# Kernel optimization log

Hardware: AMD Instinct MI355X
Metric: run time of the kernel (lower is better)

Reference implementation:

```python
import jax, jax.numpy as jnp
import numpy as np
from jax import lax

B, T, I, H, O, L = 32, 1024, 128, 512, 128, 2


def _lstm_layer(x, Wih, Whh, bih, bhh):
    # x: [B, T, in]; Wih: [4H, in]; Whh: [4H, H]; PyTorch gate order i,f,g,o
    Hs = Whh.shape[1]
    # Precompute input contribution for all timesteps (one big GEMM)
    xg = jnp.einsum('bti,gi->btg', x, Wih) + bih + bhh  # [B, T, 4H]
    xg_t = jnp.swapaxes(xg, 0, 1)  # [T, B, 4H] for scan

    def step(carry, g_in):
        h, c = carry
        g = g_in + h @ Whh.T  # [B, 4H]
        i, f, gg, o = jnp.split(g, 4, axis=-1)
        i = jax.nn.sigmoid(i)
        f = jax.nn.sigmoid(f)
        gg = jnp.tanh(gg)
        o = jax.nn.sigmoid(o)
        c = f * c + i * gg
        h = o * jnp.tanh(c)
        return (h, c), h

    h0 = jnp.zeros((x.shape[0], Hs), dtype=x.dtype)
    c0 = jnp.zeros((x.shape[0], Hs), dtype=x.dtype)
    (_, _), hs = lax.scan(step, (h0, c0), xg_t)
    return jnp.swapaxes(hs, 0, 1)  # [B, T, H]


def setup_inputs() -> dict:
    key = jax.random.key(0)
    ks = jax.random.split(key, 16)
    s = 1.0 / np.sqrt(H)  # torch LSTM/Linear init scale
    u = lambda k, shape: jax.random.uniform(k, shape, jnp.float32, -s, s)
    return {
        'x': jax.random.normal(ks[0], (B, T, I), jnp.float32),
        'W_ih0': u(ks[1], (4 * H, I)), 'W_hh0': u(ks[2], (4 * H, H)),
        'b_ih0': u(ks[3], (4 * H,)), 'b_hh0': u(ks[4], (4 * H,)),
        'W_ih1': u(ks[5], (4 * H, H)), 'W_hh1': u(ks[6], (4 * H, H)),
        'b_ih1': u(ks[7], (4 * H,)), 'b_hh1': u(ks[8], (4 * H,)),
        'fcW': u(ks[9], (O, H)), 'fcb': u(ks[10], (O,)),
        'fc2W': jax.random.uniform(ks[11], (O, O), jnp.float32, -1.0 / np.sqrt(O), 1.0 / np.sqrt(O)),
        'fc2b': jax.random.uniform(ks[12], (O,), jnp.float32, -1.0 / np.sqrt(O), 1.0 / np.sqrt(O)),
    }


def reference(x, W_ih0, W_hh0, b_ih0, b_hh0, W_ih1, W_hh1, b_ih1, b_hh1, fcW, fcb, fc2W, fc2b):
    h1 = _lstm_layer(x, W_ih0, W_hh0, b_ih0, b_hh0)   # [B, T, H]
    h2 = _lstm_layer(h1, W_ih1, W_hh1, b_ih1, b_hh1)  # [B, T, H]
    out = h2 @ fcW.T + fcb    # [B, T, O]
    out2 = out @ fc2W.T + fc2b  # [B, T, O]
    return out2
```

## Files before the change

### kernel.cpp

```cpp
#include <hip/hip_runtime.h>
#include <math.h>

typedef _Float16 f16;
typedef _Float16 f16x8 __attribute__((ext_vector_type(8)));
typedef _Float16 f16x4 __attribute__((ext_vector_type(4)));
typedef _Float16 f16x2 __attribute__((ext_vector_type(2)));
typedef float f32x16 __attribute__((ext_vector_type(16)));
typedef int i32x4 __attribute__((ext_vector_type(4)));

#define B_ 32
#define T_ 1024
#define I_ 128
#define H_ 512

#define NWG 64
#define THR 512

#define OFF_FLAGS 0UL
#define OFF_H1S   4096UL
#define OFF_H2S   33591296UL
#define OFF_XT    67178496UL

__device__ inline f32x16 mfma32(f16x8 a, f16x8 b, f32x16 c) {
  return __builtin_amdgcn_mfma_f32_32x32x16_f16(a, b, c, 0, 0, 0);
}
__device__ inline float fast_sig(float x) { return 1.f / (1.f + __expf(-x)); }
__device__ inline float fast_tanh(float x) {
  float e = __expf(-2.f * fabsf(x));
  float t = (1.f - e) / (1.f + e);
  return x < 0.f ? -t : t;
}

__device__ inline unsigned ld_sc1_u32(const unsigned* p) {
  unsigned r;
  asm volatile("global_load_dword %0, %1, off sc1\n\ts_waitcnt vmcnt(0)"
               : "=v"(r) : "v"(p) : "memory");
  return r;
}
__device__ inline void st_sc1_u32(unsigned* p, unsigned v) {
  asm volatile("global_store_dword %0, %1, off sc1" :: "v"(p), "v"(v) : "memory");
}

__device__ inline int swz_h(int b, int kbyte) { return b * 1024 + (kbyte ^ ((b & 7) << 4)); }
__device__ inline int swz_x(int b, int kbyte) { return b * 256  + (kbyte ^ ((b & 7) << 4)); }

__global__ __launch_bounds__(256) void prep_xT(const float* __restrict__ x, f16* __restrict__ xT) {
  const int idx = blockIdx.x * 256 + threadIdx.x;
  const int n4 = B_ * T_ * I_ / 4;
  if (idx < n4) {
    const int i4 = idx * 4;
    const int i  = i4 & (I_ - 1);
    const int tt = (i4 >> 7) & (T_ - 1);
    const int b  = i4 >> 17;
    float4 v = *(const float4*)(x + i4);
    f16x4 o;
    o[0] = (f16)v.x; o[1] = (f16)v.y; o[2] = (f16)v.z; o[3] = (f16)v.w;
    *(f16x4*)(xT + ((size_t)tt * B_ + b) * I_ + i) = o;
  }
}

__global__ __launch_bounds__(THR, 1) void lstm_persist(
    const float* __restrict__ Wih0, const float* __restrict__ Whh0,
    const float* __restrict__ bih0, const float* __restrict__ bhh0,
    const float* __restrict__ Wih1, const float* __restrict__ Whh1,
    const float* __restrict__ bih1, const float* __restrict__ bhh1,
    char* ws) {
  __shared__ i32x4 h1l4[2048];
  __shared__ i32x4 h2l4[2048];
  __shared__ i32x4 xl4[512];
  __shared__ float gbuf[2 * 32 * 68];
  __shared__ float biasl[64];

  const int tid  = threadIdx.x;
  const int wgid = blockIdx.x;
  const int role = wgid >> 5;
  const int gid  = wgid & 31;
  const int lane = tid & 63;
  const int wv   = tid >> 6;
  const int nt   = wv & 1;
  const int kq   = (wv >> 1) & 1;
  const int bl   = lane & 31;
  const int kg   = lane >> 5;

  unsigned* flags0 = (unsigned*)(ws + OFF_FLAGS);
  unsigned* flags1 = (unsigned*)(ws + OFF_FLAGS + 2048);
  const char* h1base = ws + OFF_H1S;
  const char* h2base = ws + OFF_H2S;

  if (tid < 64) {
    const int g = tid >> 4, hc = tid & 15;
    const int row = g * 512 + gid * 16 + hc;
    biasl[tid] = role ? (bih1[row] + bhh1[row]) : (bih0[row] + bhh0[row]);
  }

  const int n    = nt * 32 + bl;
  const int wrow = (n >> 4) * 512 + gid * 16 + (n & 15);
  f16x8 wreg[32];
  if (role == 0) {
    if (wv < 4) {
#pragma unroll
      for (int ks = 0; ks < 20; ++ks) {
        const int k = kq * 320 + ks * 16 + kg * 8;
        const float* src = (k < I_) ? (Wih0 + (size_t)wrow * I_ + k)
                                    : (Whh0 + (size_t)wrow * H_ + (k - I_));
        float4 v0 = *(const float4*)(src);
        float4 v1 = *(const float4*)(src + 4);
        f16x8 h;
        h[0] = (f16)v0.x; h[1] = (f16)v0.y; h[2] = (f16)v0.z; h[3] = (f16)v0.w;
        h[4] = (f16)v1.x; h[5] = (f16)v1.y; h[6] = (f16)v1.z; h[7] = (f16)v1.w;
        wreg[ks] = h;
      }
    }
  } else {
    if (wv < 4) {
#pragma unroll
      for (int ks = 0; ks < 32; ++ks) {
        const int k = kq * 512 + ks * 16 + kg * 8;
        const float* src = (k < H_) ? (Wih1 + (size_t)wrow * H_ + k)
                                    : (Whh1 + (size_t)wrow * H_ + (k - H_));
        float4 v0 = *(const float4*)(src);
        float4 v1 = *(const float4*)(src + 4);
        f16x8 h;
        h[0] = (f16)v0.x; h[1] = (f16)v0.y; h[2] = (f16)v0.z; h[3] = (f16)v0.w;
        h[4] = (f16)v1.x; h[5] = (f16)v1.y; h[6] = (f16)v1.z; h[7] = (f16)v1.w;
        wreg[ks] = h;
      }
    }
  }

  float cst0 = 0.f, cst1 = 0.f;
  const char* h1c = (const char*)h1l4;
  const char* h2c = (const char*)h2l4;
  const char* xc  = (const char*)xl4;

  __syncthreads();

  if (role == 0) {
    for (int s = 0; s < T_; ++s) {
      i32x4 xv = ((const i32x4*)(ws + OFF_XT))[(size_t)s * 512 + tid];

      if (s >= 1) {
        if (tid < 64) {
          const unsigned tgt = (unsigned)s;
          const unsigned* fp = flags0 + (tid < 32 ? tid : 0) * 16;
          const bool active = tid < 32;
          for (;;) {
            unsigned v = ld_sc1_u32(fp);
            if (!active) v = tgt;
            if (__all((int)(v >= tgt))) break;
            __builtin_amdgcn_s_sleep(1);
          }
        }
        __syncthreads();
      }

      {
        const i32x4* src = (const i32x4*)(h1base + (size_t)s * 32768);
#pragma unroll
        for (int r = 0; r < 4; ++r) {
          const int u = r * 512 + tid;
          i32x4 v = src[u];
          const int wgs = u >> 6, b = (u >> 1) & 31, half = u & 1;
          *(i32x4*)((char*)h1l4 + swz_h(b, wgs * 32 + half * 16)) = v;
        }
      }
      *(i32x4*)((char*)xl4 + swz_x(tid >> 4, (tid & 15) * 16)) = xv;
      __syncthreads();

      if (wv < 4) {
        f32x16 acc = {};
        if (kq == 0) {
#pragma unroll
          for (int ks = 0; ks < 8; ++ks) {
            f16x8 a = *(const f16x8*)(xc + swz_x(bl, (ks * 16 + kg * 8) * 2));
            acc = mfma32(a, wreg[ks], acc);
          }
#pragma unroll
          for (int ks = 8; ks < 20; ++ks) {
            f16x8 a = *(const f16x8*)(h1c + swz_h(bl, (ks * 16 + kg * 8 - I_) * 2));
            acc = mfma32(a, wreg[ks], acc);
          }
        } else {
#pragma unroll
          for (int ks = 0; ks < 20; ++ks) {
            f16x8 a = *(const f16x8*)(h1c + swz_h(bl, (192 + ks * 16 + kg * 8) * 2));
            acc = mfma32(a, wreg[ks], acc);
          }
        }
        const int cb = nt * 32 + bl;
#pragma unroll
        for (int r = 0; r < 16; ++r) {
          const int row = (r & 3) + 8 * (r >> 2) + 4 * kg;
          gbuf[kq * 2176 + row * 68 + cb] = acc[r];
        }
      }
      __syncthreads();

      if (tid < 256) {
        const int rb = tid >> 3, hp = tid & 7;
        const float* gr = gbuf + rb * 68;
        float hv[2];
#pragma unroll
        for (int cc = 0; cc < 2; ++cc) {
          const int c = 2 * hp + cc;
          const float pi = gr[c]      + gr[2176 + c]      + biasl[c];
          const float pf = gr[16 + c] + gr[2176 + 16 + c] + biasl[16 + c];
          const float pg = gr[32 + c] + gr[2176 + 32 + c] + biasl[32 + c];
          const float po = gr[48 + c] + gr[2176 + 48 + c] + biasl[48 + c];
          const float ig = fast_sig(pi), fg = fast_sig(pf);
          const float gg = fast_tanh(pg), og = fast_sig(po);
          const float cprev = cc ? cst1 : cst0;
          const float cnew = fg * cprev + ig * gg;
          if (cc) cst1 = cnew; else cst0 = cnew;
          hv[cc] = og * fast_tanh(cnew);
        }
        f16x2 pk; pk[0] = (f16)hv[0]; pk[1] = (f16)hv[1];
        unsigned* dst = (unsigned*)(h1base + (size_t)(s + 1) * 32768 +
                                    (size_t)gid * 1024 + rb * 32 + hp * 4);
        st_sc1_u32(dst, __builtin_bit_cast(unsigned, pk));
      }

      asm volatile("s_waitcnt vmcnt(0)" ::: "memory");
      __syncthreads();
      if (tid == 0) st_sc1_u32(flags0 + gid * 16, (unsigned)(s + 1));
      __builtin_amdgcn_sched_barrier(0);
    }
  } else {
    for (int t = 0; t < T_; ++t) {
      if (tid < 64) {
        const unsigned tgt = (unsigned)(t + 1);
        const unsigned* fp = flags0 + (tid < 32 ? tid : 0) * 16;
        const bool active = tid < 32;
        for (;;) {
          unsigned v = ld_sc1_u32(fp);
          if (!active) v = tgt;
          if (__all((int)(v >= tgt))) break;
          __builtin_amdgcn_s_sleep(1);
        }
      }
      __syncthreads();

      {
        const i32x4* src = (const i32x4*)(h1base + (size_t)(t + 1) * 32768);
#pragma unroll
        for (int r = 0; r < 4; ++r) {
          const int u = r * 512 + tid;
          i32x4 v = src[u];
          const int wgs = u >> 6, b = (u >> 1) & 31, half = u & 1;
          *(i32x4*)((char*)h1l4 + swz_h(b, wgs * 32 + half * 16)) = v;
        }
      }

      if (t >= 1) {
        if (tid < 64) {
          const unsigned tgt = (unsigned)t;
          const unsigned* fp = flags1 + (tid < 32 ? tid : 0) * 16;
          const bool active = tid < 32;
          for (;;) {
            unsigned v = ld_sc1_u32(fp);
            if (!active) v = tgt;
            if (__all((int)(v >= tgt))) break;
            __builtin_amdgcn_s_sleep(1);
          }
        }
      }
      __syncthreads();

      {
        const i32x4* src = (const i32x4*)(h2base + (size_t)t * 32768);
#pragma unroll
        for (int r = 0; r < 4; ++r) {
          const int u = r * 512 + tid;
          i32x4 v = src[u];
          const int wgs = u >> 6, b = (u >> 1) & 31, half = u & 1;
          *(i32x4*)((char*)h2l4 + swz_h(b, wgs * 32 + half * 16)) = v;
        }
      }
      __syncthreads();

      if (wv < 4) {
        f32x16 acc = {};
        if (kq == 0) {
#pragma unroll
          for (int ks = 0; ks < 32; ++ks) {
            f16x8 a = *(const f16x8*)(h1c + swz_h(bl, (ks * 16 + kg * 8) * 2));
            acc = mfma32(a, wreg[ks], acc);
          }
        } else {
#pragma unroll
          for (int ks = 0; ks < 32; ++ks) {
            f16x8 a = *(const f16x8*)(h2c + swz_h(bl, (ks * 16 + kg * 8) * 2));
            acc = mfma32(a, wreg[ks], acc);
          }
        }
        const int cb = nt * 32 + bl;
#pragma unroll
        for (int r = 0; r < 16; ++r) {
          const int row = (r & 3) + 8 * (r >> 2) + 4 * kg;
          gbuf[kq * 2176 + row * 68 + cb] = acc[r];
        }
      }
      __syncthreads();

      if (tid < 256) {
        const int rb = tid >> 3, hp = tid & 7;
        const float* gr = gbuf + rb * 68;
        float hv[2];
#pragma unroll
        for (int cc = 0; cc < 2; ++cc) {
          const int c = 2 * hp + cc;
          const float pi = gr[c]      + gr[2176 + c]      + biasl[c];
          const float pf = gr[16 + c] + gr[2176 + 16 + c] + biasl[16 + c];
          const float pg = gr[32 + c] + gr[2176 + 32 + c] + biasl[32 + c];
          const float po = gr[48 + c] + gr[2176 + 48 + c] + biasl[48 + c];
          const float ig = fast_sig(pi), fg = fast_sig(pf);
          const float gg = fast_tanh(pg), og = fast_sig(po);
          const float cprev = cc ? cst1 : cst0;
          const float cnew = fg * cprev + ig * gg;
          if (cc) cst1 = cnew; else cst0 = cnew;
          hv[cc] = og * fast_tanh(cnew);
        }
        f16x2 pk; pk[0] = (f16)hv[0]; pk[1] = (f16)hv[1];
        unsigned* dst = (unsigned*)(h2base + (size_t)(t + 1) * 32768 +
                                    (size_t)gid * 1024 + rb * 32 + hp * 4);
        st_sc1_u32(dst, __builtin_bit_cast(unsigned, pk));
      }

      asm volatile("s_waitcnt vmcnt(0)" ::: "memory");
      __syncthreads();
      if (tid == 0) st_sc1_u32(flags1 + gid * 16, (unsigned)(t + 1));
      __builtin_amdgcn_sched_barrier(0);
    }
  }
}

__global__ __launch_bounds__(256) void fc_fused(const char* __restrict__ ws_h2,
                                                const float* __restrict__ fcW,
                                                const float* __restrict__ fcb,
                                                const float* __restrict__ fc2W,
                                                const float* __restrict__ fc2b,
                                                float* __restrict__ out) {
  __shared__ float hT[64][36];
  __shared__ float wT[128][36];
  __shared__ float oL[64][136];
  const int bt0 = blockIdx.x * 64;
  const int b   = bt0 >> 10;
  const int t0  = bt0 & 1023;
  const int t = threadIdx.x;
  const int c4 = (t & 31) * 4;
  const int rowg = t >> 5;
  float acc[8][4];
#pragma unroll
  for (int r = 0; r < 8; ++r)
#pragma unroll
    for (int j = 0; j < 4; ++j) acc[r][j] = 0.f;

  for (int kc = 0; kc < 16; ++kc) {
    {
      const int r = t >> 2, q = t & 3;
      const int c0 = kc * 32 + q * 8;
      const f16x8 v = *(const f16x8*)(ws_h2 + (size_t)(t0 + r + 1) * 32768 +
                                      (size_t)(c0 >> 4) * 1024 + b * 32 + (c0 & 15) * 2);
#pragma unroll
      for (int j = 0; j < 8; ++j) hT[r][q * 8 + j] = (float)v[j];
    }
#pragma unroll
    for (int u = t; u < 1024; u += 256) {
      const int cc = u >> 3, k4 = u & 7;
      *(float4*)&wT[cc][k4 * 4] = *(const float4*)(fcW + (size_t)cc * 512 + kc * 32 + k4 * 4);
    }
    __syncthreads();
#pragma unroll
    for (int k4 = 0; k4 < 8; ++k4) {
      float4 w0 = *(float4*)&wT[c4 + 0][k4 * 4];
      float4 w1 = *(float4*)&wT[c4 + 1][k4 * 4];
      float4 w2 = *(float4*)&wT[c4 + 2][k4 * 4];
      float4 w3 = *(float4*)&wT[c4 + 3][k4 * 4];
#pragma unroll
      for (int rr = 0; rr < 8; ++rr) {
        float4 h = *(float4*)&hT[rowg * 8 + rr][k4 * 4];
        acc[rr][0] += h.x * w0.x + h.y * w0.y + h.z * w0.z + h.w * w0.w;
        acc[rr][1] += h.x * w1.x + h.y * w1.y + h.z * w1.z + h.w * w1.w;
        acc[rr][2] += h.x * w2.x + h.y * w2.y + h.z * w2.z + h.w * w2.w;
        acc[rr][3] += h.x * w3.x + h.y * w3.y + h.z * w3.z + h.w * w3.w;
      }
    }
    __syncthreads();
  }
#pragma unroll
  for (int rr = 0; rr < 8; ++rr)
#pragma unroll
    for (int j = 0; j < 4; ++j)
      oL[rowg * 8 + rr][c4 + j] = acc[rr][j] + fcb[c4 + j];
  __syncthreads();
  float a2[8][4];
#pragma unroll
  for (int r = 0; r < 8; ++r)
#pragma unroll
    for (int j = 0; j < 4; ++j) a2[r][j] = 0.f;
#pragma unroll
  for (int k4 = 0; k4 < 32; ++k4) {
    float4 w0 = *(const float4*)(fc2W + (size_t)(c4 + 0) * 128 + k4 * 4);
    float4 w1 = *(const float4*)(fc2W + (size_t)(c4 + 1) * 128 + k4 * 4);
    float4 w2 = *(const float4*)(fc2W + (size_t)(c4 + 2) * 128 + k4 * 4);
    float4 w3 = *(const float4*)(fc2W + (size_t)(c4 + 3) * 128 + k4 * 4);
#pragma unroll
    for (int rr = 0; rr < 8; ++rr) {
      float4 h = *(float4*)&oL[rowg * 8 + rr][k4 * 4];
      a2[rr][0] += h.x * w0.x + h.y * w0.y + h.z * w0.z + h.w * w0.w;
      a2[rr][1] += h.x * w1.x + h.y * w1.y + h.z * w1.z + h.w * w1.w;
      a2[rr][2] += h.x * w2.x + h.y * w2.y + h.z * w2.z + h.w * w2.w;
      a2[rr][3] += h.x * w3.x + h.y * w3.y + h.z * w3.z + h.w * w3.w;
    }
  }
#pragma unroll
  for (int rr = 0; rr < 8; ++rr) {
    const int r = bt0 + rowg * 8 + rr;
#pragma unroll
    for (int j = 0; j < 4; ++j)
      out[(size_t)r * 128 + c4 + j] = a2[rr][j] + fc2b[c4 + j];
  }
}

extern "C" void kernel_launch(void* const* d_in, const int* in_sizes, int n_in,
                              void* d_out, int out_size, void* d_ws, size_t ws_size,
                              hipStream_t stream) {
  (void)in_sizes; (void)n_in; (void)out_size; (void)ws_size;
  const float* x    = (const float*)d_in[0];
  const float* Wih0 = (const float*)d_in[1];
  const float* Whh0 = (const float*)d_in[2];
  const float* bih0 = (const float*)d_in[3];
  const float* bhh0 = (const float*)d_in[4];
  const float* Wih1 = (const float*)d_in[5];
  const float* Whh1 = (const float*)d_in[6];
  const float* bih1 = (const float*)d_in[7];
  const float* bhh1 = (const float*)d_in[8];
  const float* fcW  = (const float*)d_in[9];
  const float* fcb  = (const float*)d_in[10];
  const float* fc2W = (const float*)d_in[11];
  const float* fc2b = (const float*)d_in[12];

  char* ws = (char*)d_ws;
  f16* xT = (f16*)(ws + OFF_XT);
  float* out = (float*)d_out;

  (void)hipMemsetAsync(ws + OFF_FLAGS, 0, 4096, stream);
  (void)hipMemsetAsync(ws + OFF_H1S, 0, 32768, stream);
  (void)hipMemsetAsync(ws + OFF_H2S, 0, 32768, stream);

  prep_xT<<<4096, 256, 0, stream>>>(x, xT);
  lstm_persist<<<NWG, THR, 0, stream>>>(Wih0, Whh0, bih0, bhh0,
                                        Wih1, Whh1, bih1, bhh1, ws);
  fc_fused<<<512, 256, 0, stream>>>(ws + OFF_H2S, fcW, fcb, fc2W, fc2b, out);
}
```

Before: 3.322 ms.

## Spread LSTM gate GEMM across all eight waves and overlap layer-1 input GEMM with h2 wait

Each workgroup now splits the reduction dimension four ways across all 8 waves instead of two ways across 4 waves, halving per-wave MFMA chains and weight registers. In layer 1, the Wih1·h1 part is computed by waves 0-3 while waves 4-7 wait on the layer-1 recurrence flags and stage h2, then waves 4-7 do the Whh1·h2 part, so the input half runs off the recurrent critical path. The pointwise stage now uses all 512 threads with one element each and 16-bit stores. The cost is four partial sums to add per gate and an extra barrier phase in the layer-1 loop.

```diff
diff --git a/kernel.cpp b/kernel.cpp
--- a/kernel.cpp
+++ b/kernel.cpp
@@ -4,7 +4,6 @@
 typedef _Float16 f16;
 typedef _Float16 f16x8 __attribute__((ext_vector_type(8)));
 typedef _Float16 f16x4 __attribute__((ext_vector_type(4)));
-typedef _Float16 f16x2 __attribute__((ext_vector_type(2)));
 typedef float f32x16 __attribute__((ext_vector_type(16)));
 typedef int i32x4 __attribute__((ext_vector_type(4)));
 
@@ -20,6 +19,8 @@
 #define OFF_H1S   4096UL
 #define OFF_H2S   33591296UL
 #define OFF_XT    67178496UL
+
+#define GQ 2176
 
 __device__ inline f32x16 mfma32(f16x8 a, f16x8 b, f32x16 c) {
   return __builtin_amdgcn_mfma_f32_32x32x16_f16(a, b, c, 0, 0, 0);
@@ -39,6 +40,9 @@
 }
 __device__ inline void st_sc1_u32(unsigned* p, unsigned v) {
   asm volatile("global_store_dword %0, %1, off sc1" :: "v"(p), "v"(v) : "memory");
+}
+__device__ inline void st_sc1_u16(unsigned short* p, unsigned v) {
+  asm volatile("global_store_short %0, %1, off sc1" :: "v"(p), "v"(v) : "memory");
 }
 
 __device__ inline int swz_h(int b, int kbyte) { return b * 1024 + (kbyte ^ ((b & 7) << 4)); }
@@ -68,7 +72,7 @@
   __shared__ i32x4 h1l4[2048];
   __shared__ i32x4 h2l4[2048];
   __shared__ i32x4 xl4[512];
-  __shared__ float gbuf[2 * 32 * 68];
+  __shared__ float gbuf[4 * GQ];
   __shared__ float biasl[64];
 
   const int tid  = threadIdx.x;
@@ -77,15 +81,13 @@
   const int gid  = wgid & 31;
   const int lane = tid & 63;
   const int wv   = tid >> 6;
-  const int nt   = wv & 1;
-  const int kq   = (wv >> 1) & 1;
   const int bl   = lane & 31;
   const int kg   = lane >> 5;
 
   unsigned* flags0 = (unsigned*)(ws + OFF_FLAGS);
   unsigned* flags1 = (unsigned*)(ws + OFF_FLAGS + 2048);
-  const char* h1base = ws + OFF_H1S;
-  const char* h2base = ws + OFF_H2S;
+  char* h1b = ws + OFF_H1S;
+  char* h2b = ws + OFF_H2S;
 
   if (tid < 64) {
     const int g = tid >> 4, hc = tid & 15;
@@ -93,42 +95,42 @@
     biasl[tid] = role ? (bih1[row] + bhh1[row]) : (bih0[row] + bhh0[row]);
   }
 
-  const int n    = nt * 32 + bl;
+  const int nt = wv & 1;
+  const int n  = nt * 32 + bl;
   const int wrow = (n >> 4) * 512 + gid * 16 + (n & 15);
-  f16x8 wreg[32];
+  f16x8 wreg[16];
   if (role == 0) {
-    if (wv < 4) {
-#pragma unroll
-      for (int ks = 0; ks < 20; ++ks) {
-        const int k = kq * 320 + ks * 16 + kg * 8;
-        const float* src = (k < I_) ? (Wih0 + (size_t)wrow * I_ + k)
-                                    : (Whh0 + (size_t)wrow * H_ + (k - I_));
-        float4 v0 = *(const float4*)(src);
-        float4 v1 = *(const float4*)(src + 4);
-        f16x8 h;
-        h[0] = (f16)v0.x; h[1] = (f16)v0.y; h[2] = (f16)v0.z; h[3] = (f16)v0.w;
-        h[4] = (f16)v1.x; h[5] = (f16)v1.y; h[6] = (f16)v1.z; h[7] = (f16)v1.w;
-        wreg[ks] = h;
-      }
+    const int kp = wv >> 1;
+#pragma unroll
+    for (int ksl = 0; ksl < 10; ++ksl) {
+      const int k = kp * 160 + ksl * 16 + kg * 8;
+      const float* src = (k < I_) ? (Wih0 + (size_t)wrow * I_ + k)
+                                  : (Whh0 + (size_t)wrow * H_ + (k - I_));
+      float4 v0 = *(const float4*)(src);
+      float4 v1 = *(const float4*)(src + 4);
+      f16x8 h;
+      h[0] = (f16)v0.x; h[1] = (f16)v0.y; h[2] = (f16)v0.z; h[3] = (f16)v0.w;
+      h[4] = (f16)v1.x; h[5] = (f16)v1.y; h[6] = (f16)v1.z; h[7] = (f16)v1.w;
+      wreg[ksl] = h;
     }
   } else {
-    if (wv < 4) {
-#pragma unroll
-      for (int ks = 0; ks < 32; ++ks) {
-        const int k = kq * 512 + ks * 16 + kg * 8;
-        const float* src = (k < H_) ? (Wih1 + (size_t)wrow * H_ + k)
-                                    : (Whh1 + (size_t)wrow * H_ + (k - H_));
-        float4 v0 = *(const float4*)(src);
-        float4 v1 = *(const float4*)(src + 4);
-        f16x8 h;
-        h[0] = (f16)v0.x; h[1] = (f16)v0.y; h[2] = (f16)v0.z; h[3] = (f16)v0.w;
-        h[4] = (f16)v1.x; h[5] = (f16)v1.y; h[6] = (f16)v1.z; h[7] = (f16)v1.w;
-        wreg[ks] = h;
-      }
-    }
-  }
-
-  float cst0 = 0.f, cst1 = 0.f;
+    const int kq  = wv >> 2;
+    const int ks2 = (wv >> 1) & 1;
+#pragma unroll
+    for (int ksl = 0; ksl < 16; ++ksl) {
+      const int khalf = ks2 * 256 + ksl * 16 + kg * 8;
+      const float* src = (kq == 0) ? (Wih1 + (size_t)wrow * H_ + khalf)
+                                   : (Whh1 + (size_t)wrow * H_ + khalf);
+      float4 v0 = *(const float4*)(src);
+      float4 v1 = *(const float4*)(src + 4);
+      f16x8 h;
+      h[0] = (f16)v0.x; h[1] = (f16)v0.y; h[2] = (f16)v0.z; h[3] = (f16)v0.w;
+      h[4] = (f16)v1.x; h[5] = (f16)v1.y; h[6] = (f16)v1.z; h[7] = (f16)v1.w;
+      wreg[ksl] = h;
+    }
+  }
+
+  float cst = 0.f;
   const char* h1c = (const char*)h1l4;
   const char* h2c = (const char*)h2l4;
   const char* xc  = (const char*)xl4;
@@ -136,6 +138,7 @@
   __syncthreads();
 
   if (role == 0) {
+    const int kp = wv >> 1;
     for (int s = 0; s < T_; ++s) {
       i32x4 xv = ((const i32x4*)(ws + OFF_XT))[(size_t)s * 512 + tid];
 
@@ -155,7 +158,7 @@
       }
 
       {
-        const i32x4* src = (const i32x4*)(h1base + (size_t)s * 32768);
+        const i32x4* src = (const i32x4*)(h1b + (size_t)s * 32768);
 #pragma unroll
         for (int r = 0; r < 4; ++r) {
           const int u = r * 512 + tid;
@@ -167,57 +170,40 @@
       *(i32x4*)((char*)xl4 + swz_x(tid >> 4, (tid & 15) * 16)) = xv;
       __syncthreads();
 
-      if (wv < 4) {
+      {
         f32x16 acc = {};
-        if (kq == 0) {
-#pragma unroll
-          for (int ks = 0; ks < 8; ++ks) {
-            f16x8 a = *(const f16x8*)(xc + swz_x(bl, (ks * 16 + kg * 8) * 2));
-            acc = mfma32(a, wreg[ks], acc);
-          }
-#pragma unroll
-          for (int ks = 8; ks < 20; ++ks) {
-            f16x8 a = *(const f16x8*)(h1c + swz_h(bl, (ks * 16 + kg * 8 - I_) * 2));
-            acc = mfma32(a, wreg[ks], acc);
-          }
-        } else {
-#pragma unroll
-          for (int ks = 0; ks < 20; ++ks) {
-            f16x8 a = *(const f16x8*)(h1c + swz_h(bl, (192 + ks * 16 + kg * 8) * 2));
-            acc = mfma32(a, wreg[ks], acc);
-          }
+#pragma unroll
+        for (int ksl = 0; ksl < 10; ++ksl) {
+          const int kbase = kp * 160 + ksl * 16;
+          f16x8 a;
+          if (kbase < I_) a = *(const f16x8*)(xc + swz_x(bl, (kbase + kg * 8) * 2));
+          else            a = *(const f16x8*)(h1c + swz_h(bl, (kbase - I_ + kg * 8) * 2));
+          acc = mfma32(a, wreg[ksl], acc);
         }
         const int cb = nt * 32 + bl;
 #pragma unroll
         for (int r = 0; r < 16; ++r) {
           const int row = (r & 3) + 8 * (r >> 2) + 4 * kg;
-          gbuf[kq * 2176 + row * 68 + cb] = acc[r];
-        }
-      }
-      __syncthreads();
-
-      if (tid < 256) {
-        const int rb = tid >> 3, hp = tid & 7;
+          gbuf[kp * GQ + row * 68 + cb] = acc[r];
+        }
+      }
+      __syncthreads();
+
+      {
+        const int rb = tid >> 4, hp = tid & 15;
         const float* gr = gbuf + rb * 68;
-        float hv[2];
-#pragma unroll
-        for (int cc = 0; cc < 2; ++cc) {
-          const int c = 2 * hp + cc;
-          const float pi = gr[c]      + gr[2176 + c]      + biasl[c];
-          const float pf = gr[16 + c] + gr[2176 + 16 + c] + biasl[16 + c];
-          const float pg = gr[32 + c] + gr[2176 + 32 + c] + biasl[32 + c];
-          const float po = gr[48 + c] + gr[2176 + 48 + c] + biasl[48 + c];
-          const float ig = fast_sig(pi), fg = fast_sig(pf);
-          const float gg = fast_tanh(pg), og = fast_sig(po);
-          const float cprev = cc ? cst1 : cst0;
-          const float cnew = fg * cprev + ig * gg;
-          if (cc) cst1 = cnew; else cst0 = cnew;
-          hv[cc] = og * fast_tanh(cnew);
-        }
-        f16x2 pk; pk[0] = (f16)hv[0]; pk[1] = (f16)hv[1];
-        unsigned* dst = (unsigned*)(h1base + (size_t)(s + 1) * 32768 +
-                                    (size_t)gid * 1024 + rb * 32 + hp * 4);
-        st_sc1_u32(dst, __builtin_bit_cast(unsigned, pk));
+        const float pi = gr[hp]          + gr[GQ + hp]          + gr[2*GQ + hp]          + gr[3*GQ + hp]          + biasl[hp];
+        const float pf = gr[16 + hp]     + gr[GQ + 16 + hp]     + gr[2*GQ + 16 + hp]     + gr[3*GQ + 16 + hp]     + biasl[16 + hp];
+        const float pg = gr[32 + hp]     + gr[GQ + 32 + hp]     + gr[2*GQ + 32 + hp]     + gr[3*GQ + 32 + hp]     + biasl[32 + hp];
+        const float po = gr[48 + hp]     + gr[GQ + 48 + hp]     + gr[2*GQ + 48 + hp]     + gr[3*GQ + 48 + hp]     + biasl[48 + hp];
+        const float ig = fast_sig(pi), fg = fast_sig(pf);
+        const float gg = fast_tanh(pg), og = fast_sig(po);
+        cst = fg * cst + ig * gg;
+        const float hv = og * fast_tanh(cst);
+        const f16 hf = (f16)hv;
+        st_sc1_u16((unsigned short*)(h1b + (size_t)(s + 1) * 32768 +
+                                     (size_t)gid * 1024 + rb * 32 + hp * 2),
+                   (unsigned)__builtin_bit_cast(unsigned short, hf));
       }
 
       asm volatile("s_waitcnt vmcnt(0)" ::: "memory");
@@ -226,6 +212,7 @@
       __builtin_amdgcn_sched_barrier(0);
     }
   } else {
+    const int ks2 = (wv >> 1) & 1;
     for (int t = 0; t < T_; ++t) {
       if (tid < 64) {
         const unsigned tgt = (unsigned)(t + 1);
@@ -241,7 +228,7 @@
       __syncthreads();
 
       {
-        const i32x4* src = (const i32x4*)(h1base + (size_t)(t + 1) * 32768);
+        const i32x4* src = (const i32x4*)(h1b + (size_t)(t + 1) * 32768);
 #pragma unroll
         for (int r = 0; r < 4; ++r) {
           const int u = r * 512 + tid;
@@ -250,27 +237,37 @@
           *(i32x4*)((char*)h1l4 + swz_h(b, wgs * 32 + half * 16)) = v;
         }
       }
-
-      if (t >= 1) {
-        if (tid < 64) {
+      __syncthreads();
+
+      if (wv < 4) {
+        f32x16 acc = {};
+#pragma unroll
+        for (int ksl = 0; ksl < 16; ++ksl) {
+          f16x8 a = *(const f16x8*)(h1c + swz_h(bl, (ks2 * 256 + ksl * 16 + kg * 8) * 2));
+          acc = mfma32(a, wreg[ksl], acc);
+        }
+        const int cb = nt * 32 + bl;
+#pragma unroll
+        for (int r = 0; r < 16; ++r) {
+          const int row = (r & 3) + 8 * (r >> 2) + 4 * kg;
+          gbuf[ks2 * GQ + row * 68 + cb] = acc[r];
+        }
+      } else {
+        if (t >= 1) {
           const unsigned tgt = (unsigned)t;
-          const unsigned* fp = flags1 + (tid < 32 ? tid : 0) * 16;
-          const bool active = tid < 32;
+          const unsigned* fp = flags1 + (lane < 32 ? lane : 0) * 16;
           for (;;) {
             unsigned v = ld_sc1_u32(fp);
-            if (!active) v = tgt;
+            if (lane >= 32) v = tgt;
             if (__all((int)(v >= tgt))) break;
             __builtin_amdgcn_s_sleep(1);
           }
         }
-      }
-      __syncthreads();
-
-      {
-        const i32x4* src = (const i32x4*)(h2base + (size_t)t * 32768);
-#pragma unroll
-        for (int r = 0; r < 4; ++r) {
-          const int u = r * 512 + tid;
+        const i32x4* src = (const i32x4*)(h2b + (size_t)t * 32768);
+        const int t4 = tid - 256;
+#pragma unroll
+        for (int j = 0; j < 8; ++j) {
+          const int u = j * 256 + t4;
           i32x4 v = src[u];
           const int wgs = u >> 6, b = (u >> 1) & 31, half = u & 1;
           *(i32x4*)((char*)h2l4 + swz_h(b, wgs * 32 + half * 16)) = v;
@@ -278,52 +275,37 @@
       }
       __syncthreads();
 
-      if (wv < 4) {
+      if (wv >= 4) {
         f32x16 acc = {};
-        if (kq == 0) {
-#pragma unroll
-          for (int ks = 0; ks < 32; ++ks) {
-            f16x8 a = *(const f16x8*)(h1c + swz_h(bl, (ks * 16 + kg * 8) * 2));
-            acc = mfma32(a, wreg[ks], acc);
-          }
-        } else {
-#pragma unroll
-          for (int ks = 0; ks < 32; ++ks) {
-            f16x8 a = *(const f16x8*)(h2c + swz_h(bl, (ks * 16 + kg * 8) * 2));
-            acc = mfma32(a, wreg[ks], acc);
-          }
+#pragma unroll
+        for (int ksl = 0; ksl < 16; ++ksl) {
+          f16x8 a = *(const f16x8*)(h2c + swz_h(bl, (ks2 * 256 + ksl * 16 + kg * 8) * 2));
+          acc = mfma32(a, wreg[ksl], acc);
         }
         const int cb = nt * 32 + bl;
 #pragma unroll
         for (int r = 0; r < 16; ++r) {
           const int row = (r & 3) + 8 * (r >> 2) + 4 * kg;
-          gbuf[kq * 2176 + row * 68 + cb] = acc[r];
-        }
-      }
-      __syncthreads();
-
-      if (tid < 256) {
-        const int rb = tid >> 3, hp = tid & 7;
+          gbuf[(2 + ks2) * GQ + row * 68 + cb] = acc[r];
+        }
+      }
+      __syncthreads();
+
+      {
+        const int rb = tid >> 4, hp = tid & 15;
         const float* gr = gbuf + rb * 68;
-        float hv[2];
-#pragma unroll
-        for (int cc = 0; cc < 2; ++cc) {
-          const int c = 2 * hp + cc;
-          const float pi = gr[c]      + gr[2176 + c]      + biasl[c];
-          const float pf = gr[16 + c] + gr[2176 + 16 + c] + biasl[16 + c];
-          const float pg = gr[32 + c] + gr[2176 + 32 + c] + biasl[32 + c];
-          const float po = gr[48 + c] + gr[2176 + 48 + c] + biasl[48 + c];
-          const float ig = fast_sig(pi), fg = fast_sig(pf);
-          const float gg = fast_tanh(pg), og = fast_sig(po);
-          const float cprev = cc ? cst1 : cst0;
-          const float cnew = fg * cprev + ig * gg;
-          if (cc) cst1 = cnew; else cst0 = cnew;
-          hv[cc] = og * fast_tanh(cnew);
-        }
-        f16x2 pk; pk[0] = (f16)hv[0]; pk[1] = (f16)hv[1];
-        unsigned* dst = (unsigned*)(h2base + (size_t)(t + 1) * 32768 +
-                                    (size_t)gid * 1024 + rb * 32 + hp * 4);
-        st_sc1_u32(dst, __builtin_bit_cast(unsigned, pk));
+        const float pi = gr[hp]          + gr[GQ + hp]          + gr[2*GQ + hp]          + gr[3*GQ + hp]          + biasl[hp];
+        const float pf = gr[16 + hp]     + gr[GQ + 16 + hp]     + gr[2*GQ + 16 + hp]     + gr[3*GQ + 16 + hp]     + biasl[16 + hp];
+        const float pg = gr[32 + hp]     + gr[GQ + 32 + hp]     + gr[2*GQ + 32 + hp]     + gr[3*GQ + 32 + hp]     + biasl[32 + hp];
+        const float po = gr[48 + hp]     + gr[GQ + 48 + hp]     + gr[2*GQ + 48 + hp]     + gr[3*GQ + 48 + hp]     + biasl[48 + hp];
+        const float ig = fast_sig(pi), fg = fast_sig(pf);
+        const float gg = fast_tanh(pg), og = fast_sig(po);
+        cst = fg * cst + ig * gg;
+        const float hv = og * fast_tanh(cst);
+        const f16 hf = (f16)hv;
+        st_sc1_u16((unsigned short*)(h2b + (size_t)(t + 1) * 32768 +
+                                     (size_t)gid * 1024 + rb * 32 + hp * 2),
+                   (unsigned)__builtin_bit_cast(unsigned short, hf));
       }
 
       asm volatile("s_waitcnt vmcnt(0)" ::: "memory");
```

Result: slower. 3.496 ms (+5.2%).
